# Kernel tuning notes

Measured on AMD Instinct MI355X. Metric: run time of the kernel, lower is better.

Reference implementation:

```python
import jax, jax.numpy as jnp
import numpy as np
from jax import lax

B, CIN, COUT, H, W, K = 8, 256, 256, 64, 64, 3
KK = K * K
PAD, STRIDE = 1, 1
EPS = 1e-5


def setup_inputs() -> dict:
    key = jax.random.key(0)
    k0, k1, k2 = jax.random.split(key, 3)
    x = jax.random.normal(k0, (B, CIN, H, W), jnp.float32)
    # offset/mask predicting conv: 3*K*K output channels (o1, o2, mask)
    w_off = jax.random.normal(k1, (3 * KK, CIN, K, K), jnp.float32) * 0.01
    b_off = jnp.zeros((3 * KK,), jnp.float32)
    # main deformable conv weight
    weight = jax.random.normal(k2, (COUT, CIN, K, K), jnp.float32) / np.sqrt(CIN * KK).astype(np.float32)
    bias = jnp.zeros((COUT,), jnp.float32)
    gamma = jnp.ones((COUT,), jnp.float32)
    beta = jnp.zeros((COUT,), jnp.float32)
    return {"x": x, "w_off": w_off, "b_off": b_off, "weight": weight,
            "bias": bias, "gamma": gamma, "beta": beta}


def _bilinear_sample(img, ph, pw):
    """img: [C,H,W]; ph,pw: [KK,H,W] float sample positions. Zero outside. -> [C,KK,H,W]"""
    h0 = jnp.floor(ph).astype(jnp.int32)
    w0 = jnp.floor(pw).astype(jnp.int32)
    h1, w1 = h0 + 1, w0 + 1
    lh = ph - h0.astype(ph.dtype)
    lw = pw - w0.astype(pw.dtype)
    hh, hw = 1.0 - lh, 1.0 - lw

    def corner(hi, wi):
        valid = (hi >= 0) & (hi < H) & (wi >= 0) & (wi < W)
        hc = jnp.clip(hi, 0, H - 1)
        wc = jnp.clip(wi, 0, W - 1)
        v = img[:, hc, wc]  # [C,KK,H,W]
        return v * valid.astype(img.dtype)[None]

    return (corner(h0, w0) * (hh * hw)[None] + corner(h0, w1) * (hh * lw)[None]
            + corner(h1, w0) * (lh * hw)[None] + corner(h1, w1) * (lh * lw)[None])


def _forward(x, w_off, b_off, weight, bias, gamma, beta):
    dn = ('NCHW', 'OIHW', 'NCHW')
    # offset/mask branch (standard conv)
    om = lax.conv_general_dilated(x, w_off, (STRIDE, STRIDE), ((PAD, PAD), (PAD, PAD)),
                                  dimension_numbers=dn) + b_off[None, :, None, None]
    o1, o2, m = jnp.split(om, 3, axis=1)
    offset = jnp.concatenate([o1, o2], axis=1)          # [B, 2*KK, H, W]
    off_h = offset[:, 0::2]                             # [B, KK, H, W] dy per tap
    off_w = offset[:, 1::2]                             # [B, KK, H, W] dx per tap
    mask = jax.nn.sigmoid(m)                            # [B, KK, H, W]

    taps = jnp.arange(KK)
    base_h = (taps // K - PAD).astype(jnp.float32)[:, None, None] \
        + (jnp.arange(H, dtype=jnp.float32) * STRIDE)[None, :, None]  # [KK,H,1]
    base_w = (taps % K - PAD).astype(jnp.float32)[:, None, None] \
        + (jnp.arange(W, dtype=jnp.float32) * STRIDE)[None, None, :]  # [KK,1,W]
    ph = base_h[None] + off_h                           # [B,KK,H,W]
    pw = base_w[None] + off_w

    sampled = jax.vmap(_bilinear_sample)(x, ph, pw)     # [B,CIN,KK,H,W]
    sampled = sampled * mask[:, None]                   # modulated (DCNv2)

    y = jnp.einsum('bckhw,ock->bohw', sampled, weight.reshape(COUT, CIN, KK))
    y = y + bias[None, :, None, None]

    # BatchNorm2d (training mode: batch statistics) + ReLU
    mean = y.mean(axis=(0, 2, 3))
    var = y.var(axis=(0, 2, 3))
    yn = (y - mean[None, :, None, None]) * lax.rsqrt(var + EPS)[None, :, None, None]
    out = jax.nn.relu(gamma[None, :, None, None] * yn + beta[None, :, None, None])
    return out


def reference(x, w_off, b_off, weight, bias, gamma, beta):
    return _forward(x, w_off, b_off, weight, bias, gamma, beta)
```

## Files before the change

kernel.cpp:

```cpp
#include <hip/hip_runtime.h>
#include <cstdint>

#define BB    8
#define CIN   256
#define COUT  256
#define HH    64
#define WW    64

typedef __attribute__((ext_vector_type(8))) short    s16x8;
typedef __attribute__((ext_vector_type(8))) unsigned short u16x8;
typedef __attribute__((ext_vector_type(4))) unsigned short u16x4;
typedef __attribute__((ext_vector_type(4))) float    f32x4;

__device__ __forceinline__ float bf2f(unsigned short u) {
    unsigned int v = ((unsigned int)u) << 16;
    return __builtin_bit_cast(float, v);
}
__device__ __forceinline__ unsigned short f2bf(float f) {
    unsigned int u = __builtin_bit_cast(unsigned int, f);
    unsigned int r = (u + 0x7FFFu + ((u >> 16) & 1u)) >> 16;
    return (unsigned short)r;
}

__global__ void k_pack(const float* __restrict__ x,
                       const float* __restrict__ w,
                       const float* __restrict__ woff,
                       unsigned short* __restrict__ xT,
                       unsigned short* __restrict__ wTk,
                       unsigned short* __restrict__ wofT) {
    int blk = blockIdx.x;
    int t = threadIdx.x;
    __shared__ float tile[64 * 65];
    if (blk < 2048) {
        int b    = blk & 7;
        int rest = blk >> 3;
        int h    = rest >> 2;
        int c0   = (rest & 3) * 64;
#pragma unroll
        for (int r = 0; r < 16; ++r) {
            int idx = t + r * 256;
            int i = idx >> 6, w_ = idx & 63;
            tile[i * 65 + w_] = x[(((b * 256 + c0 + i) * 64 + h) * 64) + w_];
        }
        __syncthreads();
#pragma unroll
        for (int r = 0; r < 2; ++r) {
            int idx = t + r * 256;
            int w_ = idx >> 3;
            int c8 = (idx & 7) * 8;
            u16x8 res;
#pragma unroll
            for (int k = 0; k < 8; ++k) res[k] = f2bf(tile[(c8 + k) * 65 + w_]);
            *reinterpret_cast<u16x8*>(&xT[((b * 64 + h) * 64 + w_) * 256 + c0 + c8]) = res;
        }
    } else if (blk < 4352) {
        int idx = (blk - 2048) * 256 + t;
        int j   = idx & 7;
        int q   = (idx >> 3) & 3;
        int o16 = (idx >> 5) & 15;
        int n16 = (idx >> 9) & 15;
        int kc  = (idx >> 13) & 7;
        int tp  = idx >> 16;
        int c = kc * 32 + q * 8 + j;
        int o = n16 * 16 + o16;
        wTk[idx] = f2bf(w[(o * 256 + c) * 9 + tp]);
    } else {
        int idx = (blk - 4352) * 256 + t;
        int c  = idx & 255;
        int j  = (idx >> 8) & 31;
        int tp = idx >> 13;
        wofT[idx] = f2bf((j < 27) ? woff[(j * 256 + c) * 9 + tp] : 0.f);
    }
}

__global__ __launch_bounds__(512, 4)
void k_main(const unsigned short* __restrict__ xT,
            const unsigned short* __restrict__ wTk,
            const unsigned short* __restrict__ wofT,
            const float* __restrict__ boffg,
            const float* __restrict__ bias,
            unsigned short* __restrict__ y16,
            float* __restrict__ gsum, float* __restrict__ gssq) {
    __shared__ __align__(16) char smem[76032];
    int blk = blockIdx.x;
    int b = blk & 7, h = blk >> 3;
    int pblk = b * 64 + h;
    int t = threadIdx.x;
    int lane = t & 63, wv = t >> 6;
    int lm = lane & 15, q = lane >> 4;
    const f32x4 FZ = {0.f, 0.f, 0.f, 0.f};

    {
        unsigned short* S3 = (unsigned short*)smem;
        float* OMS = (float*)(smem + 67584);
        f32x4 oacc0 = FZ, oacc1 = FZ;
        int p0w = wv * 16;
        for (int cc = 0; cc < 2; ++cc) {
            __syncthreads();
            if (t < 96) {
                int rr = t >> 5, col = (t >> 4) & 1, c8 = (t & 15) * 8;
                u16x8 z = {0,0,0,0,0,0,0,0};
                *reinterpret_cast<u16x8*>(&S3[(rr * 66 + col * 65) * 136 + c8]) = z;
            }
#pragma unroll
            for (int r = 0; r < 6; ++r) {
                int v = t + r * 512;
                int rr = v >> 10, rem = v & 1023;
                int w_ = rem >> 4, c8 = (rem & 15) * 8;
                int hr = h + rr - 1;
                u16x8 d = {0,0,0,0,0,0,0,0};
                if (hr >= 0 && hr < 64)
                    d = *reinterpret_cast<const u16x8*>(xT + ((b * 64 + hr) * 64 + w_) * 256 + cc * 128 + c8);
                *reinterpret_cast<u16x8*>(&S3[(rr * 66 + w_ + 1) * 136 + c8]) = d;
            }
            __syncthreads();
            if (wv < 4) {
#pragma unroll
                for (int tp = 0; tp < 9; ++tp) {
                    int dh = tp / 3, dw = tp % 3;
                    const unsigned short* wb = wofT + (tp * 32 + lm) * 256 + cc * 128;
#pragma unroll
                    for (int kc = 0; kc < 4; ++kc) {
                        s16x8 a = *reinterpret_cast<const s16x8*>(
                            &S3[(dh * 66 + p0w + lm + dw) * 136 + kc * 32 + q * 8]);
                        s16x8 b0 = *reinterpret_cast<const s16x8*>(wb + kc * 32 + q * 8);
                        s16x8 b1 = *reinterpret_cast<const s16x8*>(wb + 16 * 256 + kc * 32 + q * 8);
                        oacc0 = __builtin_amdgcn_mfma_f32_16x16x32_bf16(a, b0, oacc0, 0, 0, 0);
                        oacc1 = __builtin_amdgcn_mfma_f32_16x16x32_bf16(a, b1, oacc1, 0, 0, 0);
                    }
                }
            }
        }
        if (wv < 4) {
#pragma unroll
            for (int n = 0; n < 2; ++n) {
                int j = n * 16 + lm;
                float bj = (j < 27) ? boffg[j] : 0.f;
                f32x4 a = n ? oacc1 : oacc0;
#pragma unroll
                for (int i = 0; i < 4; ++i)
                    OMS[(p0w + q * 4 + i) * 33 + j] = a[i] + bj;
            }
        }
        __syncthreads();
    }

    unsigned short* S = (unsigned short*)smem;
    float* OMS = (float*)(smem + 67584);
    f32x4 acc[4][4];
#pragma unroll
    for (int m = 0; m < 4; ++m)
#pragma unroll
        for (int n = 0; n < 4; ++n) acc[m][n] = FZ;

    if (wv >= 4) {
        int pw = wv - 4;
        int s  = lane & 7;
        int pA = pw * 16 + (lane >> 3);
        int pB = pA + 8;
        int rb = b * 4096;

        float wgA[4], wgB[4];
        int   adA[4], adB[4];

        auto setup = [&](int tp, int p, float* wgt, int* ad) {
            float oh = OMS[p * 33 + 2 * tp];
            float ow = OMS[p * 33 + 2 * tp + 1];
            float mv = OMS[p * 33 + 18 + tp];
            float mk = 1.f / (1.f + __expf(-mv));
            float ph = (float)(h + tp / 3 - 1) + oh;
            float pw_ = (float)(p + tp % 3 - 1) + ow;
            float fh0 = floorf(ph), fw0 = floorf(pw_);
            int ih0 = (int)fh0, iw0 = (int)fw0;
            float lh = ph - fh0, lw = pw_ - fw0;
            float hh = 1.f - lh, hw_ = 1.f - lw;
            bool vh0 = (ih0 >= 0) & (ih0 < 64);
            bool vh1 = (ih0 + 1 >= 0) & (ih0 + 1 < 64);
            bool vw0 = (iw0 >= 0) & (iw0 < 64);
            bool vw1 = (iw0 + 1 >= 0) & (iw0 + 1 < 64);
            wgt[0] = hh * hw_ * mk * (float)(vh0 & vw0);
            wgt[1] = hh * lw  * mk * (float)(vh0 & vw1);
            wgt[2] = lh * hw_ * mk * (float)(vh1 & vw0);
            wgt[3] = lh * lw  * mk * (float)(vh1 & vw1);
            int ch0 = min(max(ih0, 0), 63), ch1 = min(max(ih0 + 1, 0), 63);
            int cw0 = min(max(iw0, 0), 63), cw1 = min(max(iw0 + 1, 0), 63);
            ad[0] = ((rb + ch0 * 64 + cw0) * 256);
            ad[1] = ((rb + ch0 * 64 + cw1) * 256);
            ad[2] = ((rb + ch1 * 64 + cw0) * 256);
            ad[3] = ((rb + ch1 * 64 + cw1) * 256);
        };

        u16x8 rP[4], rQ[4];
        auto issueSet = [&](const int* ad, int j, u16x8* r) {
            int off = j * 64 + s * 8;
#pragma unroll
            for (int c = 0; c < 4; ++c)
                r[c] = *reinterpret_cast<const u16x8*>(xT + ad[c] + off);
        };
        auto blendSet = [&](int buf, int p, const float* wgt, int j, u16x8* r) {
            u16x8 res;
#pragma unroll
            for (int k = 0; k < 8; ++k) {
                float v = wgt[0] * bf2f(r[0][k]);
                v = fmaf(wgt[1], bf2f(r[1][k]), v);
                v = fmaf(wgt[2], bf2f(r[2][k]), v);
                v = fmaf(wgt[3], bf2f(r[3][k]), v);
                res[k] = f2bf(v);
            }
            *reinterpret_cast<u16x8*>(&S[buf * 16896 + p * 264 + j * 64 + s * 8]) = res;
        };
        auto fillTap = [&](int tp, int buf) {
            setup(tp, pA, wgA, adA);
            setup(tp, pB, wgB, adB);
            issueSet(adA, 0, rP);
            issueSet(adA, 1, rQ);
            blendSet(buf, pA, wgA, 0, rP);  issueSet(adA, 2, rP);
            blendSet(buf, pA, wgA, 1, rQ);  issueSet(adA, 3, rQ);
            blendSet(buf, pA, wgA, 2, rP);  issueSet(adB, 0, rP);
            blendSet(buf, pA, wgA, 3, rQ);  issueSet(adB, 1, rQ);
            blendSet(buf, pB, wgB, 0, rP);  issueSet(adB, 2, rP);
            blendSet(buf, pB, wgB, 1, rQ);  issueSet(adB, 3, rQ);
            blendSet(buf, pB, wgB, 2, rP);
            blendSet(buf, pB, wgB, 3, rQ);
        };

        fillTap(0, 0);
        __syncthreads();
        for (int tp = 0; tp < 9; ++tp) {
            if (tp < 8) fillTap(tp + 1, (tp + 1) & 1);
            __syncthreads();
        }
    } else {
        __syncthreads();
        for (int tp = 0; tp < 9; ++tp) {
            const unsigned short* Sc = &S[(tp & 1) * 16896];
            const unsigned short* wtap = wTk + (size_t)tp * 65536
                                       + (size_t)(wv * 4) * 512 + lm * 32 + q * 8;
            s16x8 wbuf[2][4];
#pragma unroll
            for (int n = 0; n < 4; ++n)
                wbuf[0][n] = *reinterpret_cast<const s16x8*>(wtap + n * 512);
#pragma unroll
            for (int kc = 0; kc < 8; ++kc) {
                if (kc < 7) {
                    const unsigned short* wb = wtap + (kc + 1) * 8192;
#pragma unroll
                    for (int n = 0; n < 4; ++n)
                        wbuf[(kc + 1) & 1][n] = *reinterpret_cast<const s16x8*>(wb + n * 512);
                }
#pragma unroll
                for (int mt = 0; mt < 4; ++mt) {
                    s16x8 a = *reinterpret_cast<const s16x8*>(
                        &Sc[(mt * 16 + lm) * 264 + kc * 32 + q * 8]);
#pragma unroll
                    for (int n = 0; n < 4; ++n)
                        acc[mt][n] = __builtin_amdgcn_mfma_f32_16x16x32_bf16(
                            a, wbuf[kc & 1][n], acc[mt][n], 0, 0, 0);
                }
            }
            __syncthreads();
        }
    }

    if (wv < 4) {
        u16x4* yv = reinterpret_cast<u16x4*>(y16);
#pragma unroll
        for (int nt = 0; nt < 4; ++nt) {
            int o = wv * 64 + nt * 16 + lm;
            float bo = bias[o];
            float sacc = 0.f, ssacc = 0.f;
#pragma unroll
            for (int mt = 0; mt < 4; ++mt) {
                u16x4 st;
#pragma unroll
                for (int i = 0; i < 4; ++i) {
                    float v = acc[mt][nt][i] + bo;
                    st[i] = f2bf(v);
                    sacc += v; ssacc += v * v;
                }
                int idx4 = ((pblk * 4 + wv) * 16 + nt * 4 + mt) * 64 + lane;
                yv[idx4] = st;
            }
            sacc  += __shfl_xor(sacc, 16);
            sacc  += __shfl_xor(sacc, 32);
            ssacc += __shfl_xor(ssacc, 16);
            ssacc += __shfl_xor(ssacc, 32);
            if (q == 0) {
                atomicAdd(&gsum[o], sacc);
                atomicAdd(&gssq[o], ssacc);
            }
        }
    }
}

__global__ void k_bnrelu(const unsigned short* __restrict__ y16,
                         const float* __restrict__ gsum, const float* __restrict__ gssq,
                         const float* __restrict__ gamma, const float* __restrict__ beta,
                         float* __restrict__ out) {
    int blk = blockIdx.x;
    int b = blk & 7, h = blk >> 3;
    int pblk = b * 64 + h;
    __shared__ unsigned short T[64 * 257];
    __shared__ float sc[256], sh[256];
    int t = threadIdx.x;
    {
        const float n = 32768.f;
        float mean = gsum[t] / n;
        float var = gssq[t] / n - mean * mean;
        float inv = rsqrtf(var + 1e-5f);
        float s = gamma[t] * inv;
        sc[t] = s;
        sh[t] = beta[t] - mean * s;
    }
    const u16x4* yv = reinterpret_cast<const u16x4*>(y16) + pblk * 4096;
#pragma unroll
    for (int r = 0; r < 16; ++r) {
        int v = t + r * 256;
        u16x4 d = yv[v];
        int lane = v & 63, mt = (v >> 6) & 3, nt = (v >> 8) & 3, wvv = (v >> 10) & 3;
        int p = mt * 16 + (lane >> 4) * 4;
        int o = wvv * 64 + nt * 16 + (lane & 15);
        T[(p + 0) * 257 + o] = d[0];
        T[(p + 1) * 257 + o] = d[1];
        T[(p + 2) * 257 + o] = d[2];
        T[(p + 3) * 257 + o] = d[3];
    }
    __syncthreads();
    int w4   = (t & 15) * 4;
    int orow = t >> 4;
    float* obase = out + (size_t)b * (256 * 4096) + h * 64;
#pragma unroll
    for (int it = 0; it < 16; ++it) {
        int o = orow + it * 16;
        float scl = sc[o], shf = sh[o];
        float4 vo;
        vo.x = fmaxf(bf2f(T[(w4 + 0) * 257 + o]) * scl + shf, 0.f);
        vo.y = fmaxf(bf2f(T[(w4 + 1) * 257 + o]) * scl + shf, 0.f);
        vo.z = fmaxf(bf2f(T[(w4 + 2) * 257 + o]) * scl + shf, 0.f);
        vo.w = fmaxf(bf2f(T[(w4 + 3) * 257 + o]) * scl + shf, 0.f);
        *reinterpret_cast<float4*>(obase + (size_t)o * 4096 + w4) = vo;
    }
}

extern "C" void kernel_launch(void* const* d_in, const int* in_sizes, int n_in,
                              void* d_out, int out_size, void* d_ws, size_t ws_size,
                              hipStream_t stream) {
    const float* x      = (const float*)d_in[0];
    const float* w_off  = (const float*)d_in[1];
    const float* b_off  = (const float*)d_in[2];
    const float* weight = (const float*)d_in[3];
    const float* bias   = (const float*)d_in[4];
    const float* gamma  = (const float*)d_in[5];
    const float* beta   = (const float*)d_in[6];

    char* ws = (char*)d_ws;
    const size_t OFF_XT    = 0;
    const size_t OFF_WT    = OFF_XT + 16777216;
    const size_t OFF_WOFT  = OFF_WT + 1179648;
    const size_t OFF_Y16   = OFF_WOFT + 147456;
    const size_t OFF_SUM   = OFF_Y16 + 16777216;
    const size_t OFF_SUMSQ = OFF_SUM + 1024;

    unsigned short* xT   = (unsigned short*)(ws + OFF_XT);
    unsigned short* wTk  = (unsigned short*)(ws + OFF_WT);
    unsigned short* wofT = (unsigned short*)(ws + OFF_WOFT);
    unsigned short* y16  = (unsigned short*)(ws + OFF_Y16);
    float* gsum  = (float*)(ws + OFF_SUM);
    float* gssq  = (float*)(ws + OFF_SUMSQ);

    hipMemsetAsync(ws + OFF_SUM, 0, 2048, stream);

    k_pack  <<<4640, 256, 0, stream>>>(x, weight, w_off, xT, wTk, wofT);
    k_main  <<< 512, 512, 0, stream>>>(xT, wTk, wofT, b_off, bias, y16, gsum, gssq);
    k_bnrelu<<< 512, 256, 0, stream>>>(y16, gsum, gssq, gamma, beta, (float*)d_out);
}
```

Measured before the change: 207.2 us.

## Fuse pack, conv and BN-ReLU into one persistent kernel with grid barriers

Merges the three kernels into a single 512-block launch that uses atomic-counter grid barriers between the pack, main conv and BN/ReLU phases. The conv result stays in shared memory across the second barrier instead of going through a bf16 global buffer, which removes one round trip to global memory and two launches. Weights are packed into per-batch replicas so that all blocks share the packing work. The change relies on all 512 blocks being co-resident (4 per CU at 512 threads), otherwise the spin barriers deadlock, and the busy-wait plus the extra replica writes add cost.

```diff
diff --git a/kernel.cpp b/kernel.cpp
--- a/kernel.cpp
+++ b/kernel.cpp
@@ -9,7 +9,6 @@
 
 typedef __attribute__((ext_vector_type(8))) short    s16x8;
 typedef __attribute__((ext_vector_type(8))) unsigned short u16x8;
-typedef __attribute__((ext_vector_type(4))) unsigned short u16x4;
 typedef __attribute__((ext_vector_type(4))) float    f32x4;
 
 __device__ __forceinline__ float bf2f(unsigned short u) {
@@ -22,73 +21,88 @@
     return (unsigned short)r;
 }
 
-__global__ void k_pack(const float* __restrict__ x,
-                       const float* __restrict__ w,
-                       const float* __restrict__ woff,
-                       unsigned short* __restrict__ xT,
-                       unsigned short* __restrict__ wTk,
-                       unsigned short* __restrict__ wofT) {
-    int blk = blockIdx.x;
-    int t = threadIdx.x;
-    __shared__ float tile[64 * 65];
-    if (blk < 2048) {
-        int b    = blk & 7;
-        int rest = blk >> 3;
-        int h    = rest >> 2;
-        int c0   = (rest & 3) * 64;
-#pragma unroll
-        for (int r = 0; r < 16; ++r) {
-            int idx = t + r * 256;
-            int i = idx >> 6, w_ = idx & 63;
-            tile[i * 65 + w_] = x[(((b * 256 + c0 + i) * 64 + h) * 64) + w_];
-        }
-        __syncthreads();
-#pragma unroll
-        for (int r = 0; r < 2; ++r) {
-            int idx = t + r * 256;
-            int w_ = idx >> 3;
-            int c8 = (idx & 7) * 8;
-            u16x8 res;
-#pragma unroll
-            for (int k = 0; k < 8; ++k) res[k] = f2bf(tile[(c8 + k) * 65 + w_]);
-            *reinterpret_cast<u16x8*>(&xT[((b * 64 + h) * 64 + w_) * 256 + c0 + c8]) = res;
-        }
-    } else if (blk < 4352) {
-        int idx = (blk - 2048) * 256 + t;
-        int j   = idx & 7;
-        int q   = (idx >> 3) & 3;
-        int o16 = (idx >> 5) & 15;
-        int n16 = (idx >> 9) & 15;
-        int kc  = (idx >> 13) & 7;
-        int tp  = idx >> 16;
-        int c = kc * 32 + q * 8 + j;
-        int o = n16 * 16 + o16;
-        wTk[idx] = f2bf(w[(o * 256 + c) * 9 + tp]);
-    } else {
-        int idx = (blk - 4352) * 256 + t;
-        int c  = idx & 255;
-        int j  = (idx >> 8) & 31;
-        int tp = idx >> 13;
-        wofT[idx] = f2bf((j < 27) ? woff[(j * 256 + c) * 9 + tp] : 0.f);
-    }
+__device__ __forceinline__ void grid_sync(int* cnt, int t) {
+    __syncthreads();
+    if (t == 0) {
+        __threadfence();
+        atomicAdd(cnt, 1);
+        while (__hip_atomic_load(cnt, __ATOMIC_ACQUIRE, __HIP_MEMORY_SCOPE_AGENT) < 512) {}
+        __threadfence();
+    }
+    __syncthreads();
 }
 
 __global__ __launch_bounds__(512, 4)
-void k_main(const unsigned short* __restrict__ xT,
-            const unsigned short* __restrict__ wTk,
-            const unsigned short* __restrict__ wofT,
-            const float* __restrict__ boffg,
-            const float* __restrict__ bias,
-            unsigned short* __restrict__ y16,
-            float* __restrict__ gsum, float* __restrict__ gssq) {
+void k_all(const float* __restrict__ xg,
+           const float* __restrict__ woffg,
+           const float* __restrict__ boffg,
+           const float* __restrict__ wg,
+           const float* __restrict__ biasg,
+           const float* __restrict__ gammag,
+           const float* __restrict__ betag,
+           unsigned short* __restrict__ xT,
+           unsigned short* __restrict__ wTkAll,
+           unsigned short* __restrict__ wofTAll,
+           float* __restrict__ gsum,
+           float* __restrict__ gssq,
+           int* __restrict__ cnt,
+           float* __restrict__ out) {
     __shared__ __align__(16) char smem[76032];
     int blk = blockIdx.x;
     int b = blk & 7, h = blk >> 3;
-    int pblk = b * 64 + h;
     int t = threadIdx.x;
     int lane = t & 63, wv = t >> 6;
     int lm = lane & 15, q = lane >> 4;
     const f32x4 FZ = {0.f, 0.f, 0.f, 0.f};
+
+    unsigned short* wTk  = wTkAll  + (size_t)b * 589824;
+    unsigned short* wofT = wofTAll + (size_t)b * 73728;
+
+    {
+        int k = blk >> 3;
+        for (int r = 0; r < 18; ++r) {
+            int idx = k * 9216 + r * 512 + t;
+            int j   = idx & 7;
+            int qq  = (idx >> 3) & 3;
+            int o16 = (idx >> 5) & 15;
+            int n16 = (idx >> 9) & 15;
+            int kc  = (idx >> 13) & 7;
+            int tp  = idx >> 16;
+            int c = kc * 32 + qq * 8 + j;
+            int o = n16 * 16 + o16;
+            wTk[idx] = f2bf(wg[(o * 256 + c) * 9 + tp]);
+        }
+        for (int r = 0; r < 3; ++r) {
+            int j2 = r * 512 + t;
+            if (j2 < 1152) {
+                int idx = k * 1152 + j2;
+                int c  = idx & 255;
+                int j  = (idx >> 8) & 31;
+                int tp = idx >> 13;
+                wofT[idx] = f2bf((j < 27) ? woffg[(j * 256 + c) * 9 + tp] : 0.f);
+            }
+        }
+        float* tileF = (float*)smem;
+        for (int cq = 0; cq < 4; ++cq) {
+            int c0 = cq * 64;
+            __syncthreads();
+#pragma unroll
+            for (int r = 0; r < 8; ++r) {
+                int idx = t + r * 512;
+                int i = idx >> 6, w_ = idx & 63;
+                tileF[i * 65 + w_] = xg[(((b * 256 + c0 + i) * 64 + h) * 64) + w_];
+            }
+            __syncthreads();
+            {
+                int w_ = t >> 3, c8 = (t & 7) * 8;
+                u16x8 res;
+#pragma unroll
+                for (int kk = 0; kk < 8; ++kk) res[kk] = f2bf(tileF[(c8 + kk) * 65 + w_]);
+                *reinterpret_cast<u16x8*>(&xT[((b * 64 + h) * 64 + w_) * 256 + c0 + c8]) = res;
+            }
+        }
+    }
+    grid_sync(&cnt[0], t);
 
     {
         unsigned short* S3 = (unsigned short*)smem;
@@ -262,24 +276,22 @@
         }
     }
 
+    __syncthreads();
+    unsigned short* T = (unsigned short*)smem;
     if (wv < 4) {
-        u16x4* yv = reinterpret_cast<u16x4*>(y16);
 #pragma unroll
         for (int nt = 0; nt < 4; ++nt) {
             int o = wv * 64 + nt * 16 + lm;
-            float bo = bias[o];
+            float bo = biasg[o];
             float sacc = 0.f, ssacc = 0.f;
 #pragma unroll
             for (int mt = 0; mt < 4; ++mt) {
-                u16x4 st;
 #pragma unroll
                 for (int i = 0; i < 4; ++i) {
                     float v = acc[mt][nt][i] + bo;
-                    st[i] = f2bf(v);
+                    T[(mt * 16 + q * 4 + i) * 257 + o] = f2bf(v);
                     sacc += v; ssacc += v * v;
                 }
-                int idx4 = ((pblk * 4 + wv) * 16 + nt * 4 + mt) * 64 + lane;
-                yv[idx4] = st;
             }
             sacc  += __shfl_xor(sacc, 16);
             sacc  += __shfl_xor(sacc, 32);
@@ -291,47 +303,27 @@
             }
         }
     }
-}
-
-__global__ void k_bnrelu(const unsigned short* __restrict__ y16,
-                         const float* __restrict__ gsum, const float* __restrict__ gssq,
-                         const float* __restrict__ gamma, const float* __restrict__ beta,
-                         float* __restrict__ out) {
-    int blk = blockIdx.x;
-    int b = blk & 7, h = blk >> 3;
-    int pblk = b * 64 + h;
-    __shared__ unsigned short T[64 * 257];
-    __shared__ float sc[256], sh[256];
-    int t = threadIdx.x;
-    {
-        const float n = 32768.f;
-        float mean = gsum[t] / n;
-        float var = gssq[t] / n - mean * mean;
+    grid_sync(&cnt[1], t);
+
+    float* sc = (float*)(smem + 67584);
+    float* sh = sc + 256;
+    if (t < 256) {
+        const float invn = 1.f / 32768.f;
+        float s_  = __hip_atomic_load(&gsum[t], __ATOMIC_ACQUIRE, __HIP_MEMORY_SCOPE_AGENT);
+        float ss_ = __hip_atomic_load(&gssq[t], __ATOMIC_ACQUIRE, __HIP_MEMORY_SCOPE_AGENT);
+        float mean = s_ * invn;
+        float var = ss_ * invn - mean * mean;
         float inv = rsqrtf(var + 1e-5f);
-        float s = gamma[t] * inv;
-        sc[t] = s;
-        sh[t] = beta[t] - mean * s;
-    }
-    const u16x4* yv = reinterpret_cast<const u16x4*>(y16) + pblk * 4096;
-#pragma unroll
-    for (int r = 0; r < 16; ++r) {
-        int v = t + r * 256;
-        u16x4 d = yv[v];
-        int lane = v & 63, mt = (v >> 6) & 3, nt = (v >> 8) & 3, wvv = (v >> 10) & 3;
-        int p = mt * 16 + (lane >> 4) * 4;
-        int o = wvv * 64 + nt * 16 + (lane & 15);
-        T[(p + 0) * 257 + o] = d[0];
-        T[(p + 1) * 257 + o] = d[1];
-        T[(p + 2) * 257 + o] = d[2];
-        T[(p + 3) * 257 + o] = d[3];
+        float g = gammag[t] * inv;
+        sc[t] = g;
+        sh[t] = betag[t] - mean * g;
     }
     __syncthreads();
-    int w4   = (t & 15) * 4;
-    int orow = t >> 4;
     float* obase = out + (size_t)b * (256 * 4096) + h * 64;
 #pragma unroll
-    for (int it = 0; it < 16; ++it) {
-        int o = orow + it * 16;
+    for (int r = 0; r < 8; ++r) {
+        int idx = t + r * 512;
+        int o = idx >> 4, w4 = (idx & 15) * 4;
         float scl = sc[o], shf = sh[o];
         float4 vo;
         vo.x = fmaxf(bf2f(T[(w4 + 0) * 257 + o]) * scl + shf, 0.f);
@@ -356,21 +348,21 @@
     char* ws = (char*)d_ws;
     const size_t OFF_XT    = 0;
     const size_t OFF_WT    = OFF_XT + 16777216;
-    const size_t OFF_WOFT  = OFF_WT + 1179648;
-    const size_t OFF_Y16   = OFF_WOFT + 147456;
-    const size_t OFF_SUM   = OFF_Y16 + 16777216;
+    const size_t OFF_WOFT  = OFF_WT + 9437184;
+    const size_t OFF_SUM   = OFF_WOFT + 1179648;
     const size_t OFF_SUMSQ = OFF_SUM + 1024;
+    const size_t OFF_CNT   = OFF_SUMSQ + 1024;
 
     unsigned short* xT   = (unsigned short*)(ws + OFF_XT);
     unsigned short* wTk  = (unsigned short*)(ws + OFF_WT);
     unsigned short* wofT = (unsigned short*)(ws + OFF_WOFT);
-    unsigned short* y16  = (unsigned short*)(ws + OFF_Y16);
-    float* gsum  = (float*)(ws + OFF_SUM);
-    float* gssq  = (float*)(ws + OFF_SUMSQ);
-
-    hipMemsetAsync(ws + OFF_SUM, 0, 2048, stream);
-
-    k_pack  <<<4640, 256, 0, stream>>>(x, weight, w_off, xT, wTk, wofT);
-    k_main  <<< 512, 512, 0, stream>>>(xT, wTk, wofT, b_off, bias, y16, gsum, gssq);
-    k_bnrelu<<< 512, 256, 0, stream>>>(y16, gsum, gssq, gamma, beta, (float*)d_out);
-}
+    float* gsum = (float*)(ws + OFF_SUM);
+    float* gssq = (float*)(ws + OFF_SUMSQ);
+    int*   cnt  = (int*)(ws + OFF_CNT);
+    float* outp = (float*)d_out;
+
+    hipMemsetAsync(ws + OFF_SUM, 0, 2048 + 128, stream);
+
+    k_all<<<512, 512, 0, stream>>>(x, w_off, b_off, weight, bias, gamma, beta,
+                                   xT, wTk, wofT, gsum, gssq, cnt, outp);
+}
```

Result: slower. 366.3 us (+76.8%).
